# Kernel optimization log

Measured on AMD Instinct MI355X. Metric: run time of the kernel, lower is better.

Reference implementation:

```python
import jax, jax.numpy as jnp
import numpy as np

NUM_CLS = 80
C = 256
IMG = 1024.0
N = 256
SR = 2  # sampling_ratio
MIN_SIZE = 16.0
SCALES = (0.25, 0.125, 0.0625, 0.03125)
HW = ((256, 256), (128, 128), (64, 64), (32, 32))


def _roialign(feat, rois, scale, out):
    # feat: [C, H, W]; rois: [n, 4] (y1, x1, y2, x2) in image coords.
    # torchvision-style ROIAlign (aligned=False), sampling_ratio=SR, avg pool.
    Cc, H, W = feat.shape
    n = rois.shape[0]
    y1 = rois[:, 0] * scale
    x1 = rois[:, 1] * scale
    rh = jnp.maximum(rois[:, 2] * scale - y1, 1.0)
    rw = jnp.maximum(rois[:, 3] * scale - x1, 1.0)
    # per-bin sample offsets: (bin + (s+0.5)/SR) * bin_size
    g = (jnp.arange(out, dtype=feat.dtype)[:, None]
         + (jnp.arange(SR, dtype=feat.dtype)[None, :] + 0.5) / SR).reshape(-1)  # [out*SR]
    ys = y1[:, None] + g[None, :] * (rh / out)[:, None]  # [n, out*SR]
    xs = x1[:, None] + g[None, :] * (rw / out)[:, None]
    S = out * SR
    yy = jnp.broadcast_to(ys[:, :, None], (n, S, S)).reshape(n, S * S)
    xx = jnp.broadcast_to(xs[:, None, :], (n, S, S)).reshape(n, S * S)
    valid = (yy > -1.0) & (yy < H) & (xx > -1.0) & (xx < W)
    yc = jnp.clip(yy, 0.0, H - 1.0)
    xc = jnp.clip(xx, 0.0, W - 1.0)
    y0 = jnp.floor(yc)
    x0 = jnp.floor(xc)
    ly = yc - y0
    lx = xc - x0
    y0i = y0.astype(jnp.int32)
    x0i = x0.astype(jnp.int32)
    y1i = jnp.minimum(y0i + 1, H - 1)
    x1i = jnp.minimum(x0i + 1, W - 1)
    f00 = feat[:, y0i, x0i]  # [C, n, S*S]
    f01 = feat[:, y0i, x1i]
    f10 = feat[:, y1i, x0i]
    f11 = feat[:, y1i, x1i]
    val = (f00 * (1 - ly) * (1 - lx) + f01 * (1 - ly) * lx
           + f10 * ly * (1 - lx) + f11 * ly * lx)
    val = jnp.where(valid[None], val, 0.0)
    val = val.reshape(Cc, n, out, SR, out, SR).mean(axis=(3, 5))
    return val.transpose(1, 0, 2, 3)  # [n, C, out, out]


def _pool(P, rois, out):
    # roi_layer: FPN level assignment via log2 of sqrt(area)/224, clamp to levels 0..3
    area = jnp.prod(rois[:, 2:4] - rois[:, 0:2] + 1.0, axis=-1)
    lvl = jnp.clip(jnp.floor(4.0 + jnp.log(jnp.sqrt(area) / 224.0) / np.log(2.0)), 2.0, 5.0) - 2.0
    lvl = lvl.astype(jnp.int32)
    pooled = jnp.zeros((rois.shape[0], C, out, out), dtype=rois.dtype)
    for l in range(4):
        pl = _roialign(P[l], rois, SCALES[l], out)
        pooled = pooled + jnp.where((lvl == l)[:, None, None, None], pl, 0.0)
    return pooled


def _loc2bbox(loc, anchor):
    chw = anchor[..., 2:4] - anchor[..., 0:2]
    cyx = anchor[..., 0:2] + chw * 0.5
    yx = loc[..., 0:2] * chw + cyx
    hw = jnp.exp(loc[..., 2:4]) * chw
    return jnp.concatenate([yx - hw * 0.5, yx + hw * 0.5], axis=-1)


def _head(x, W1, b1, W2, b2, Wc, bc, Wl, bl):
    x = x.reshape(x.shape[0], -1)
    h = jax.nn.relu(x @ W1 + b1)
    h = jax.nn.relu(h @ W2 + b2)
    return h @ Wc + bc, h @ Wl + bl


def _cascade(P, rois, params):
    stds = (jnp.array([0.1, 0.1, 0.2, 0.2], dtype=rois.dtype),
            jnp.array([0.05, 0.05, 0.1, 0.1], dtype=rois.dtype),
            jnp.array([1 / 30.0, 1 / 30.0, 1 / 15.0, 1 / 15.0], dtype=rois.dtype))
    roi = rois
    valid = jnp.ones((rois.shape[0],), dtype=bool)
    t = jnp.arange(rois.shape[0])
    pre_b = jnp.zeros((rois.shape[0], NUM_CLS, 4), dtype=rois.dtype)
    pre_s = jnp.zeros((rois.shape[0], NUM_CLS), dtype=rois.dtype)
    for s in range(3):
        x = _pool(P, roi, 7)
        logits, loc = _head(x, *params[s])
        loc = loc.reshape(-1, NUM_CLS + 1, 4)[:, 1:] * stds[s]
        boxes = _loc2bbox(loc, roi[:, None, :])  # [N, NUM_CLS, 4]
        score = jax.nn.softmax(logits, axis=-1)[:, 1:]
        pre_b = pre_b + boxes
        pre_s = pre_s + score
        best = jnp.argmax(score, axis=-1)
        roi = boxes[t, best]
        roi = jnp.clip(roi, 0.0, IMG)  # square image: clamp both coords to [0, IMG]
        if s < 2:  # original filters only after stages 1 and 2
            hw = roi[:, 2:4] - roi[:, 0:2]
            valid = valid & jnp.all(hw >= MIN_SIZE, axis=-1)
    m = valid.astype(pre_s.dtype)
    return pre_b / 3.0 * m[:, None, None], pre_s / 3.0 * m[:, None]


def setup_inputs():
    key = jax.random.key(0)
    ks = jax.random.split(key, 32)
    inp = {}
    for i, (h, w) in enumerate(HW):
        inp[f"P{i}"] = jax.random.normal(ks[i], (C, h, w), dtype=jnp.float32)
    yx1 = jax.random.uniform(ks[4], (N, 2), minval=0.0, maxval=IMG - 64.0)
    sz = jnp.exp(jax.random.uniform(ks[5], (N, 2), minval=np.log(16.0), maxval=np.log(600.0)))
    yx2 = jnp.clip(yx1 + sz, 0.0, IMG - 1.0)
    inp["rois"] = jnp.concatenate([yx1, yx2], axis=-1).astype(jnp.float32)
    dims = [(C * 49, 1024), (1024,), (1024, 1024), (1024,),
            (1024, NUM_CLS + 1), (NUM_CLS + 1,), (1024, (NUM_CLS + 1) * 4), ((NUM_CLS + 1) * 4,)]
    names = ["W1", "b1", "W2", "b2", "Wc", "bc", "Wl", "bl"]
    k = 6
    for s in range(3):
        for nm, d in zip(names, dims):
            if len(d) == 1:
                inp[f"s{s}_{nm}"] = jnp.zeros(d, dtype=jnp.float32)
            else:
                inp[f"s{s}_{nm}"] = 0.02 * jax.random.normal(ks[k], d, dtype=jnp.float32)
                k += 1
    return inp


def reference(P0, P1, P2, P3, rois,
              s0_W1, s0_b1, s0_W2, s0_b2, s0_Wc, s0_bc, s0_Wl, s0_bl,
              s1_W1, s1_b1, s1_W2, s1_b2, s1_Wc, s1_bc, s1_Wl, s1_bl,
              s2_W1, s2_b1, s2_W2, s2_b2, s2_Wc, s2_bc, s2_Wl, s2_bl):
    P = (P0, P1, P2, P3)
    params = [(s0_W1, s0_b1, s0_W2, s0_b2, s0_Wc, s0_bc, s0_Wl, s0_bl),
              (s1_W1, s1_b1, s1_W2, s1_b2, s1_Wc, s1_bc, s1_Wl, s1_bl),
              (s2_W1, s2_b1, s2_W2, s2_b2, s2_Wc, s2_bc, s2_Wl, s2_bl)]
    return _cascade(P, rois, params)
```

## Files before the change

kernel.cpp:

```cpp
#include <hip/hip_runtime.h>
#include <math.h>


#define NROI 256
#define NCLS 80
#define APITCH 40

typedef __attribute__((ext_vector_type(8))) short short8;
typedef __attribute__((ext_vector_type(4))) float f32x4;

__device__ __forceinline__ unsigned short f2bf(float f) {
  unsigned u = __builtin_bit_cast(unsigned, f);
  unsigned r = (u + 0x7FFFu + ((u >> 16) & 1u)) >> 16;
  return (unsigned short)r;
}
__device__ __forceinline__ float bf2f(unsigned short u) {
  return __builtin_bit_cast(float, (unsigned)u << 16);
}

__global__ __launch_bounds__(256) void init_kernel(const float* __restrict__ rois,
                                                   float* __restrict__ roi,
                                                   float* __restrict__ valid) {
  int i = blockIdx.x * 256 + threadIdx.x;
  if (i < NROI * 4) roi[i] = rois[i];
  if (i < NROI) valid[i] = 1.0f;
}

__global__ __launch_bounds__(256) void transpose_bf16(const float* __restrict__ W,
                                                      unsigned short* __restrict__ Wt,
                                                      int K, int N) {
  __shared__ unsigned short tile[32][33];
  int t = threadIdx.x;
  int k0 = blockIdx.x * 32;
  int n0 = blockIdx.y * 32;
  int r = t >> 3;
  int c4 = (t & 7) * 4;
  float4 v = *(const float4*)(W + (size_t)(k0 + r) * N + n0 + c4);
  tile[r][c4 + 0] = f2bf(v.x);
  tile[r][c4 + 1] = f2bf(v.y);
  tile[r][c4 + 2] = f2bf(v.z);
  tile[r][c4 + 3] = f2bf(v.w);
  __syncthreads();
  struct __attribute__((aligned(8))) US4 { unsigned short a, b, c, d; } o;
  o.a = tile[c4 + 0][r];
  o.b = tile[c4 + 1][r];
  o.c = tile[c4 + 2][r];
  o.d = tile[c4 + 3][r];
  *(US4*)(Wt + (size_t)(n0 + r) * K + k0 + c4) = o;
}

__global__ __launch_bounds__(256) void transpose_w1(const float* __restrict__ W,
                                                    unsigned short* __restrict__ Wt) {
  __shared__ unsigned short tile[32][33];
  int t = threadIdx.x;
  int kd0 = blockIdx.x * 32;
  int n0 = blockIdx.y * 32;
  int p = kd0 >> 8;
  int c0 = kd0 & 255;
  int r = t >> 3;
  int c4 = (t & 7) * 4;
  int k_src = (c0 + r) * 49 + p;
  float4 v = *(const float4*)(W + (size_t)k_src * 1024 + n0 + c4);
  tile[r][c4 + 0] = f2bf(v.x);
  tile[r][c4 + 1] = f2bf(v.y);
  tile[r][c4 + 2] = f2bf(v.z);
  tile[r][c4 + 3] = f2bf(v.w);
  __syncthreads();
  struct __attribute__((aligned(8))) US4 { unsigned short a, b, c, d; } o;
  o.a = tile[c4 + 0][r];
  o.b = tile[c4 + 1][r];
  o.c = tile[c4 + 2][r];
  o.d = tile[c4 + 3][r];
  *(US4*)(Wt + (size_t)(n0 + r) * 12544 + kd0 + c4) = o;
}

__global__ __launch_bounds__(256) void head_transpose(const float* __restrict__ Wc,
                                                      const float* __restrict__ Wl,
                                                      unsigned short* __restrict__ Wt) {
  __shared__ unsigned short tile[32][33];
  int t = threadIdx.x;
  int k0 = blockIdx.x * 32;
  int n0 = blockIdx.y * 32;
  int r = t >> 3;
  int c4 = (t & 7) * 4;
#pragma unroll
  for (int j = 0; j < 4; j++) {
    int nn = n0 + c4 + j;
    float v = 0.0f;
    if (nn < 81) v = Wc[(size_t)(k0 + r) * 81 + nn];
    else if (nn < 405) v = Wl[(size_t)(k0 + r) * 324 + (nn - 81)];
    tile[r][c4 + j] = f2bf(v);
  }
  __syncthreads();
  struct __attribute__((aligned(8))) US4 { unsigned short a, b, c, d; } o;
  o.a = tile[c4 + 0][r];
  o.b = tile[c4 + 1][r];
  o.c = tile[c4 + 2][r];
  o.d = tile[c4 + 3][r];
  *(US4*)(Wt + (size_t)(n0 + r) * 1024 + k0 + c4) = o;
}

__global__ __launch_bounds__(256) void pool_kernel2(
    const unsigned short* __restrict__ Pb0, const unsigned short* __restrict__ Pb1,
    const unsigned short* __restrict__ Pb2, const unsigned short* __restrict__ Pb3,
    const float* __restrict__ roi, unsigned short* __restrict__ pooled) {
  int t = threadIdx.x;
  int n = blockIdx.y;
  int p = blockIdx.x * 4 + (t >> 6);
  if (p >= 49) return;
  int lane = t & 63;
  int c4 = lane * 4;
  int py = p / 7, px = p % 7;

  float r0 = roi[n * 4 + 0];
  float r1 = roi[n * 4 + 1];
  float r2 = roi[n * 4 + 2];
  float r3 = roi[n * 4 + 3];

  float area = (r2 - r0 + 1.0f) * (r3 - r1 + 1.0f);
  float lf = floorf(4.0f + log2f(sqrtf(area) / 224.0f));
  lf = fminf(fmaxf(lf, 2.0f), 5.0f);
  int lvl = (int)lf - 2;

  float scale;
  int H;
  const unsigned short* fb;
  if (lvl == 0)      { scale = 0.25f;    H = 256; fb = Pb0; }
  else if (lvl == 1) { scale = 0.125f;   H = 128; fb = Pb1; }
  else if (lvl == 2) { scale = 0.0625f;  H = 64;  fb = Pb2; }
  else               { scale = 0.03125f; H = 32;  fb = Pb3; }
  int W = H;

  float y1 = r0 * scale;
  float x1 = r1 * scale;
  float rh = fmaxf(r2 * scale - y1, 1.0f);
  float rw = fmaxf(r3 * scale - x1, 1.0f);
  float bh = rh * (1.0f / 7.0f);
  float bw = rw * (1.0f / 7.0f);

  float a0 = 0.f, a1 = 0.f, a2 = 0.f, a3 = 0.f;
#pragma unroll
  for (int ry = 0; ry < 2; ry++) {
    float yy = y1 + ((float)py + ((float)ry + 0.5f) * 0.5f) * bh;
    bool vy = (yy > -1.0f) && (yy < (float)H);
    float ycl = fminf(fmaxf(yy, 0.0f), (float)(H - 1));
    float y0f = floorf(ycl);
    float ly = ycl - y0f;
    int y0i = (int)y0f;
    int y1i = min(y0i + 1, H - 1);
#pragma unroll
    for (int rx = 0; rx < 2; rx++) {
      float xx = x1 + ((float)px + ((float)rx + 0.5f) * 0.5f) * bw;
      bool vx = (xx > -1.0f) && (xx < (float)W);
      float xcl = fminf(fmaxf(xx, 0.0f), (float)(W - 1));
      float x0f = floorf(xcl);
      float lx = xcl - x0f;
      int x0i = (int)x0f;
      int x1i = min(x0i + 1, W - 1);
      float w00 = (1.f - ly) * (1.f - lx);
      float w01 = (1.f - ly) * lx;
      float w10 = ly * (1.f - lx);
      float w11 = ly * lx;
      if (!(vy && vx)) { w00 = w01 = w10 = w11 = 0.f; }
      ushort4 f00 = *(const ushort4*)(fb + ((size_t)(y0i * W + x0i) * 256 + c4));
      ushort4 f01 = *(const ushort4*)(fb + ((size_t)(y0i * W + x1i) * 256 + c4));
      ushort4 f10 = *(const ushort4*)(fb + ((size_t)(y1i * W + x0i) * 256 + c4));
      ushort4 f11 = *(const ushort4*)(fb + ((size_t)(y1i * W + x1i) * 256 + c4));
      a0 += bf2f(f00.x) * w00 + bf2f(f01.x) * w01 + bf2f(f10.x) * w10 + bf2f(f11.x) * w11;
      a1 += bf2f(f00.y) * w00 + bf2f(f01.y) * w01 + bf2f(f10.y) * w10 + bf2f(f11.y) * w11;
      a2 += bf2f(f00.z) * w00 + bf2f(f01.z) * w01 + bf2f(f10.z) * w10 + bf2f(f11.z) * w11;
      a3 += bf2f(f00.w) * w00 + bf2f(f01.w) * w01 + bf2f(f10.w) * w10 + bf2f(f11.w) * w11;
    }
  }
  ushort4 o;
  o.x = f2bf(a0 * 0.25f);
  o.y = f2bf(a1 * 0.25f);
  o.z = f2bf(a2 * 0.25f);
  o.w = f2bf(a3 * 0.25f);
  *(ushort4*)(pooled + (size_t)n * 12544 + p * 256 + c4) = o;
}

__global__ __launch_bounds__(256) void gemm_bf16(
    const unsigned short* __restrict__ A, const unsigned short* __restrict__ B,
    float* __restrict__ Cpart, int M, int N, int K, int iters) {
  __shared__ unsigned short As[128 * APITCH];
  __shared__ unsigned short Bs[128 * APITCH];
  const int t = threadIdx.x;
  const int n0 = blockIdx.x * 128;
  const int m0 = blockIdx.y * 128;
  const size_t kt0 = (size_t)blockIdx.z * iters * 32;

  const int row = t >> 2;
  const int off = (t & 3) * 8;
  const unsigned short* pa0 = A + (size_t)(m0 + row) * K + kt0 + off;
  const unsigned short* pa1 = pa0 + (size_t)64 * K;
  const unsigned short* pb0 = B + (size_t)(n0 + row) * K + kt0 + off;
  const unsigned short* pb1 = pb0 + (size_t)64 * K;

  const int lane = t & 63;
  const int wave = t >> 6;
  const int wm = (wave >> 1) * 64;
  const int wn = (wave & 1) * 64;
  const int fr = lane & 15;
  const int kq = (lane >> 4) * 8;

  f32x4 acc[4][4];
#pragma unroll
  for (int i = 0; i < 4; i++)
#pragma unroll
    for (int j = 0; j < 4; j++) acc[i][j] = (f32x4){0.f, 0.f, 0.f, 0.f};

  uint4 ra0 = *(const uint4*)pa0;
  uint4 ra1 = *(const uint4*)pa1;
  uint4 rb0 = *(const uint4*)pb0;
  uint4 rb1 = *(const uint4*)pb1;

  for (int it = 0; it < iters; ++it) {
    *(uint4*)&As[row * APITCH + off] = ra0;
    *(uint4*)&As[(row + 64) * APITCH + off] = ra1;
    *(uint4*)&Bs[row * APITCH + off] = rb0;
    *(uint4*)&Bs[(row + 64) * APITCH + off] = rb1;
    __syncthreads();
    if (it + 1 < iters) {
      int d = (it + 1) * 32;
      ra0 = *(const uint4*)(pa0 + d);
      ra1 = *(const uint4*)(pa1 + d);
      rb0 = *(const uint4*)(pb0 + d);
      rb1 = *(const uint4*)(pb1 + d);
    }
    short8 af[4], bfv[4];
#pragma unroll
    for (int f = 0; f < 4; f++)
      af[f] = *(const short8*)&As[(wm + f * 16 + fr) * APITCH + kq];
#pragma unroll
    for (int f = 0; f < 4; f++)
      bfv[f] = *(const short8*)&Bs[(wn + f * 16 + fr) * APITCH + kq];
#pragma unroll
    for (int fm = 0; fm < 4; fm++)
#pragma unroll
      for (int fn = 0; fn < 4; fn++)
        acc[fm][fn] = __builtin_amdgcn_mfma_f32_16x16x32_bf16(af[fm], bfv[fn],
                                                              acc[fm][fn], 0, 0, 0);
    __syncthreads();
  }

  float* Cp = Cpart + (size_t)blockIdx.z * M * N;
  const int colb = n0 + wn + fr;
  const int rowb = m0 + wm + (lane >> 4) * 4;
#pragma unroll
  for (int fm = 0; fm < 4; fm++)
#pragma unroll
    for (int fn = 0; fn < 4; fn++)
#pragma unroll
      for (int r = 0; r < 4; r++)
        Cp[(size_t)(rowb + fm * 16 + r) * N + (colb + fn * 16)] = acc[fm][fn][r];
}

__global__ __launch_bounds__(256) void reduce_bias_relu(
    const float* __restrict__ parts, int nparts, const float* __restrict__ bias,
    unsigned short* __restrict__ outb) {
  int i = blockIdx.x * 256 + threadIdx.x;
  float s = 0.0f;
  for (int p = 0; p < nparts; ++p) s += parts[(size_t)p * 262144 + i];
  s = fmaxf(s + bias[i & 1023], 0.0f);
  outb[i] = f2bf(s);
}

__global__ __launch_bounds__(128) void decode_kernel(
    const float* __restrict__ headp, const float* __restrict__ bc,
    const float* __restrict__ bl,
    float* __restrict__ roi, float* __restrict__ valid,
    float* __restrict__ pre_b, float* __restrict__ pre_s,
    float st0, float st1, float st2, float st3, int stage) {
  int n = blockIdx.x;
  int t = threadIdx.x;
  __shared__ float red[128];
  __shared__ int redi[128];
  __shared__ float sroi[4];
  __shared__ float boxes[NCLS][4];

  if (t < 4) sroi[t] = roi[n * 4 + t];
  float l = -INFINITY;
  if (t < 81) {
    float s = 0.f;
#pragma unroll
    for (int z = 0; z < 4; z++) s += headp[(size_t)z * 131072 + n * 512 + t];
    l = s + bc[t];
  }
  red[t] = l;
  __syncthreads();
#pragma unroll
  for (int s = 64; s > 0; s >>= 1) {
    if (t < s) red[t] = fmaxf(red[t], red[t + s]);
    __syncthreads();
  }
  float mx = red[0];
  __syncthreads();
  red[t] = (t < 81) ? expf(l - mx) : 0.0f;
  __syncthreads();
#pragma unroll
  for (int s = 64; s > 0; s >>= 1) {
    if (t < s) red[t] += red[t + s];
    __syncthreads();
  }
  float denom = red[0];
  __syncthreads();

  float score = -INFINITY;
  if (t < NCLS) {
    float lj = 0.f;
#pragma unroll
    for (int z = 0; z < 4; z++) lj += headp[(size_t)z * 131072 + n * 512 + (t + 1)];
    lj += bc[t + 1];
    score = expf(lj - mx) / denom;
    float lp[4];
#pragma unroll
    for (int j = 0; j < 4; j++) {
      float s = 0.f;
#pragma unroll
      for (int z = 0; z < 4; z++)
        s += headp[(size_t)z * 131072 + n * 512 + 81 + (t + 1) * 4 + j];
      lp[j] = s + bl[(t + 1) * 4 + j];
    }
    float dy = lp[0] * st0;
    float dx = lp[1] * st1;
    float dh = lp[2] * st2;
    float dw = lp[3] * st3;
    float h_ = sroi[2] - sroi[0];
    float w_ = sroi[3] - sroi[1];
    float cy = sroi[0] + h_ * 0.5f;
    float cx = sroi[1] + w_ * 0.5f;
    float ny = dy * h_ + cy;
    float nx = dx * w_ + cx;
    float nh = expf(dh) * h_;
    float nw = expf(dw) * w_;
    float b0 = ny - nh * 0.5f;
    float b1v = nx - nw * 0.5f;
    float b2v = ny + nh * 0.5f;
    float b3v = nx + nw * 0.5f;
    int o = (n * NCLS + t) * 4;
    pre_b[o + 0] += b0;
    pre_b[o + 1] += b1v;
    pre_b[o + 2] += b2v;
    pre_b[o + 3] += b3v;
    pre_s[n * NCLS + t] += score;
    boxes[t][0] = b0;
    boxes[t][1] = b1v;
    boxes[t][2] = b2v;
    boxes[t][3] = b3v;
  }
  red[t] = score;
  redi[t] = t;
  __syncthreads();
  for (int s = 64; s > 0; s >>= 1) {
    if (t < s) {
      float o2 = red[t + s];
      int oi = redi[t + s];
      if (o2 > red[t] || (o2 == red[t] && oi < redi[t])) {
        red[t] = o2;
        redi[t] = oi;
      }
    }
    __syncthreads();
  }
  if (t == 0) {
    int best = redi[0];
    float ry1 = fminf(fmaxf(boxes[best][0], 0.0f), 1024.0f);
    float rx1 = fminf(fmaxf(boxes[best][1], 0.0f), 1024.0f);
    float ry2 = fminf(fmaxf(boxes[best][2], 0.0f), 1024.0f);
    float rx2 = fminf(fmaxf(boxes[best][3], 0.0f), 1024.0f);
    roi[n * 4 + 0] = ry1;
    roi[n * 4 + 1] = rx1;
    roi[n * 4 + 2] = ry2;
    roi[n * 4 + 3] = rx2;
    if (stage < 2) {
      float hh = ry2 - ry1, ww = rx2 - rx1;
      if (!(hh >= 16.0f && ww >= 16.0f)) valid[n] = 0.0f;
    }
  }
}

__global__ __launch_bounds__(256) void finalize_kernel(
    const float* __restrict__ pre_b, const float* __restrict__ pre_s,
    const float* __restrict__ valid, float* __restrict__ out) {
  int i = blockIdx.x * 256 + threadIdx.x;
  if (i < NROI * NCLS * 4) {
    int n = i / (NCLS * 4);
    out[i] = pre_b[i] * valid[n] * (1.0f / 3.0f);
  } else if (i < NROI * NCLS * 4 + NROI * NCLS) {
    int j = i - NROI * NCLS * 4;
    int n = j / NCLS;
    out[i] = pre_s[j] * valid[n] * (1.0f / 3.0f);
  }
}

extern "C" void kernel_launch(void* const* d_in, const int* in_sizes, int n_in,
                              void* d_out, int out_size, void* d_ws, size_t ws_size,
                              hipStream_t stream) {
  const float* P0 = (const float*)d_in[0];
  const float* P1 = (const float*)d_in[1];
  const float* P2 = (const float*)d_in[2];
  const float* P3 = (const float*)d_in[3];
  const float* rois = (const float*)d_in[4];
  float* out = (float*)d_out;
  float* ws = (float*)d_ws;

  float* roi   = ws;
  float* valid = roi + 1024;
  float* pre_b = valid + 256;
  float* pre_s = pre_b + 81920;
  float* part1 = pre_s + 20480;
  float* part2 = part1 + 14 * 262144;
  float* parth = part2 + 8 * 262144;
  unsigned short* pooledb = (unsigned short*)(parth + 4 * 131072);
  unsigned short* Wt1 = pooledb + (size_t)256 * 12544;
  unsigned short* Wt2 = Wt1 + (size_t)1024 * 12544;
  unsigned short* Wth = Wt2 + (size_t)1024 * 1024;
  unsigned short* h1b = Wth + (size_t)512 * 1024;
  unsigned short* h2b = h1b + (size_t)256 * 1024;
  unsigned short* Pb0 = h2b + (size_t)256 * 1024;
  unsigned short* Pb1 = Pb0 + (size_t)65536 * 256;
  unsigned short* Pb2 = Pb1 + (size_t)16384 * 256;
  unsigned short* Pb3 = Pb2 + (size_t)4096 * 256;

  init_kernel<<<4, 256, 0, stream>>>(rois, roi, valid);
  hipMemsetAsync(pre_b, 0, (size_t)(81920 + 20480) * sizeof(float), stream);

  transpose_bf16<<<dim3(8, 2048), 256, 0, stream>>>(P0, Pb0, 256, 65536);
  transpose_bf16<<<dim3(8, 512),  256, 0, stream>>>(P1, Pb1, 256, 16384);
  transpose_bf16<<<dim3(8, 128),  256, 0, stream>>>(P2, Pb2, 256, 4096);
  transpose_bf16<<<dim3(8, 32),   256, 0, stream>>>(P3, Pb3, 256, 1024);

  const float stds[3][4] = {
      {0.1f, 0.1f, 0.2f, 0.2f},
      {0.05f, 0.05f, 0.1f, 0.1f},
      {1.0f / 30.0f, 1.0f / 30.0f, 1.0f / 15.0f, 1.0f / 15.0f}};

  for (int s = 0; s < 3; s++) {
    const float* W1 = (const float*)d_in[5 + s * 8 + 0];
    const float* b1 = (const float*)d_in[5 + s * 8 + 1];
    const float* W2 = (const float*)d_in[5 + s * 8 + 2];
    const float* b2 = (const float*)d_in[5 + s * 8 + 3];
    const float* Wc = (const float*)d_in[5 + s * 8 + 4];
    const float* bc = (const float*)d_in[5 + s * 8 + 5];
    const float* Wl = (const float*)d_in[5 + s * 8 + 6];
    const float* bl = (const float*)d_in[5 + s * 8 + 7];

    transpose_w1<<<dim3(392, 32), 256, 0, stream>>>(W1, Wt1);
    transpose_bf16<<<dim3(32, 32), 256, 0, stream>>>(W2, Wt2, 1024, 1024);
    head_transpose<<<dim3(32, 16), 256, 0, stream>>>(Wc, Wl, Wth);

    pool_kernel2<<<dim3(13, 256), 256, 0, stream>>>(Pb0, Pb1, Pb2, Pb3, roi, pooledb);

    gemm_bf16<<<dim3(8, 2, 14), 256, 0, stream>>>(pooledb, Wt1, part1, 256, 1024, 12544, 28);
    reduce_bias_relu<<<1024, 256, 0, stream>>>(part1, 14, b1, h1b);

    gemm_bf16<<<dim3(8, 2, 8), 256, 0, stream>>>(h1b, Wt2, part2, 256, 1024, 1024, 4);
    reduce_bias_relu<<<1024, 256, 0, stream>>>(part2, 8, b2, h2b);

    gemm_bf16<<<dim3(4, 2, 4), 256, 0, stream>>>(h2b, Wth, parth, 256, 512, 1024, 8);

    decode_kernel<<<256, 128, 0, stream>>>(parth, bc, bl, roi, valid, pre_b, pre_s,
                                           stds[s][0], stds[s][1], stds[s][2], stds[s][3], s);
  }

  finalize_kernel<<<400, 256, 0, stream>>>(pre_b, pre_s, valid, out);
}
```

Before: 505.7 us.

## Batch all weight/feature prep into two kernels and fuse FC2 bias-ReLU epilogue

Hoists the per-stage weight transposes for all three stages into one prep kernel launched up front, together with ROI init and zeroing, and merges the four feature-map transposes into one kernel. This cuts kernel launch count and removes the per-stage serialization of transpose work. The second FC GEMM drops split-K and fuses bias plus ReLU into its epilogue, which removes the partial buffer and a reduce kernel. In exchange, the FC2 GEMM now runs on only 16 blocks with the full K loop, so it exposes much less parallelism, and the workspace must hold three sets of transposed weights.

```diff
diff --git a/kernel.cpp b/kernel.cpp
--- a/kernel.cpp
+++ b/kernel.cpp
@@ -8,6 +8,8 @@
 
 typedef __attribute__((ext_vector_type(8))) short short8;
 typedef __attribute__((ext_vector_type(4))) float f32x4;
+
+struct __attribute__((aligned(8))) US4 { unsigned short a, b, c, d; };
 
 __device__ __forceinline__ unsigned short f2bf(float f) {
   unsigned u = __builtin_bit_cast(unsigned, f);
@@ -18,86 +20,115 @@
   return __builtin_bit_cast(float, (unsigned)u << 16);
 }
 
-__global__ __launch_bounds__(256) void init_kernel(const float* __restrict__ rois,
-                                                   float* __restrict__ roi,
-                                                   float* __restrict__ valid) {
-  int i = blockIdx.x * 256 + threadIdx.x;
-  if (i < NROI * 4) roi[i] = rois[i];
-  if (i < NROI) valid[i] = 1.0f;
-}
-
-__global__ __launch_bounds__(256) void transpose_bf16(const float* __restrict__ W,
-                                                      unsigned short* __restrict__ Wt,
-                                                      int K, int N) {
+struct PrepArgs {
+  const float* W1[3];
+  const float* W2[3];
+  const float* Wc[3];
+  const float* Wl[3];
+  unsigned short* Wt1[3];
+  unsigned short* Wt2[3];
+  unsigned short* Wth[3];
+  const float* rois;
+  float* roi;
+  float* valid;
+  float* zero_base;
+  int zero_count;
+};
+
+__global__ __launch_bounds__(256) void prep_all(PrepArgs a) {
   __shared__ unsigned short tile[32][33];
-  int t = threadIdx.x;
-  int k0 = blockIdx.x * 32;
-  int n0 = blockIdx.y * 32;
+  const int b = blockIdx.x;
+  const int t = threadIdx.x;
+  const int r = t >> 3;
+  const int c4 = (t & 7) * 4;
+
+  if (b < 37632) {
+    int s = b / 12544;
+    int tau = b % 12544;
+    int kd0 = (tau % 392) * 32;
+    int n0 = (tau / 392) * 32;
+    int p = kd0 >> 8;
+    int c0 = kd0 & 255;
+    int k_src = (c0 + r) * 49 + p;
+    float4 v = *(const float4*)(a.W1[s] + (size_t)k_src * 1024 + n0 + c4);
+    tile[r][c4 + 0] = f2bf(v.x);
+    tile[r][c4 + 1] = f2bf(v.y);
+    tile[r][c4 + 2] = f2bf(v.z);
+    tile[r][c4 + 3] = f2bf(v.w);
+    __syncthreads();
+    US4 o = {tile[c4 + 0][r], tile[c4 + 1][r], tile[c4 + 2][r], tile[c4 + 3][r]};
+    *(US4*)(a.Wt1[s] + (size_t)(n0 + r) * 12544 + kd0 + c4) = o;
+  } else if (b < 40704) {
+    int bb = b - 37632;
+    int s = bb / 1024;
+    int tau = bb % 1024;
+    int k0 = (tau % 32) * 32;
+    int n0 = (tau / 32) * 32;
+    float4 v = *(const float4*)(a.W2[s] + (size_t)(k0 + r) * 1024 + n0 + c4);
+    tile[r][c4 + 0] = f2bf(v.x);
+    tile[r][c4 + 1] = f2bf(v.y);
+    tile[r][c4 + 2] = f2bf(v.z);
+    tile[r][c4 + 3] = f2bf(v.w);
+    __syncthreads();
+    US4 o = {tile[c4 + 0][r], tile[c4 + 1][r], tile[c4 + 2][r], tile[c4 + 3][r]};
+    *(US4*)(a.Wt2[s] + (size_t)(n0 + r) * 1024 + k0 + c4) = o;
+  } else if (b < 42240) {
+    int bb = b - 40704;
+    int s = bb / 512;
+    int tau = bb % 512;
+    int k0 = (tau % 32) * 32;
+    int n0 = (tau / 32) * 32;
+#pragma unroll
+    for (int j = 0; j < 4; j++) {
+      int nn = n0 + c4 + j;
+      float v = 0.0f;
+      if (nn < 81) v = a.Wc[s][(size_t)(k0 + r) * 81 + nn];
+      else if (nn < 405) v = a.Wl[s][(size_t)(k0 + r) * 324 + (nn - 81)];
+      tile[r][c4 + j] = f2bf(v);
+    }
+    __syncthreads();
+    US4 o = {tile[c4 + 0][r], tile[c4 + 1][r], tile[c4 + 2][r], tile[c4 + 3][r]};
+    *(US4*)(a.Wth[s] + (size_t)(n0 + r) * 1024 + k0 + c4) = o;
+  } else if (b == 42240) {
+    for (int i = t; i < NROI * 4; i += 256) a.roi[i] = a.rois[i];
+    a.valid[t] = 1.0f;
+  } else {
+    int base = (b - 42241) * 1024 + t;
+#pragma unroll
+    for (int j = 0; j < 4; j++) {
+      int ii = base + j * 256;
+      if (ii < a.zero_count) a.zero_base[ii] = 0.0f;
+    }
+  }
+}
+
+__global__ __launch_bounds__(256) void feat_all(
+    const float* __restrict__ P0, const float* __restrict__ P1,
+    const float* __restrict__ P2, const float* __restrict__ P3,
+    unsigned short* __restrict__ Pb0, unsigned short* __restrict__ Pb1,
+    unsigned short* __restrict__ Pb2, unsigned short* __restrict__ Pb3) {
+  __shared__ unsigned short tile[32][33];
+  const int b = blockIdx.x;
+  const int t = threadIdx.x;
+  const float* src;
+  unsigned short* dst;
+  int N, tau;
+  if (b < 16384)      { src = P0; dst = Pb0; N = 65536; tau = b; }
+  else if (b < 20480) { src = P1; dst = Pb1; N = 16384; tau = b - 16384; }
+  else if (b < 21504) { src = P2; dst = Pb2; N = 4096;  tau = b - 20480; }
+  else                { src = P3; dst = Pb3; N = 1024;  tau = b - 21504; }
+  int k0 = (tau & 7) * 32;
+  int n0 = (tau >> 3) * 32;
   int r = t >> 3;
   int c4 = (t & 7) * 4;
-  float4 v = *(const float4*)(W + (size_t)(k0 + r) * N + n0 + c4);
+  float4 v = *(const float4*)(src + (size_t)(k0 + r) * N + n0 + c4);
   tile[r][c4 + 0] = f2bf(v.x);
   tile[r][c4 + 1] = f2bf(v.y);
   tile[r][c4 + 2] = f2bf(v.z);
   tile[r][c4 + 3] = f2bf(v.w);
   __syncthreads();
-  struct __attribute__((aligned(8))) US4 { unsigned short a, b, c, d; } o;
-  o.a = tile[c4 + 0][r];
-  o.b = tile[c4 + 1][r];
-  o.c = tile[c4 + 2][r];
-  o.d = tile[c4 + 3][r];
-  *(US4*)(Wt + (size_t)(n0 + r) * K + k0 + c4) = o;
-}
-
-__global__ __launch_bounds__(256) void transpose_w1(const float* __restrict__ W,
-                                                    unsigned short* __restrict__ Wt) {
-  __shared__ unsigned short tile[32][33];
-  int t = threadIdx.x;
-  int kd0 = blockIdx.x * 32;
-  int n0 = blockIdx.y * 32;
-  int p = kd0 >> 8;
-  int c0 = kd0 & 255;
-  int r = t >> 3;
-  int c4 = (t & 7) * 4;
-  int k_src = (c0 + r) * 49 + p;
-  float4 v = *(const float4*)(W + (size_t)k_src * 1024 + n0 + c4);
-  tile[r][c4 + 0] = f2bf(v.x);
-  tile[r][c4 + 1] = f2bf(v.y);
-  tile[r][c4 + 2] = f2bf(v.z);
-  tile[r][c4 + 3] = f2bf(v.w);
-  __syncthreads();
-  struct __attribute__((aligned(8))) US4 { unsigned short a, b, c, d; } o;
-  o.a = tile[c4 + 0][r];
-  o.b = tile[c4 + 1][r];
-  o.c = tile[c4 + 2][r];
-  o.d = tile[c4 + 3][r];
-  *(US4*)(Wt + (size_t)(n0 + r) * 12544 + kd0 + c4) = o;
-}
-
-__global__ __launch_bounds__(256) void head_transpose(const float* __restrict__ Wc,
-                                                      const float* __restrict__ Wl,
-                                                      unsigned short* __restrict__ Wt) {
-  __shared__ unsigned short tile[32][33];
-  int t = threadIdx.x;
-  int k0 = blockIdx.x * 32;
-  int n0 = blockIdx.y * 32;
-  int r = t >> 3;
-  int c4 = (t & 7) * 4;
-#pragma unroll
-  for (int j = 0; j < 4; j++) {
-    int nn = n0 + c4 + j;
-    float v = 0.0f;
-    if (nn < 81) v = Wc[(size_t)(k0 + r) * 81 + nn];
-    else if (nn < 405) v = Wl[(size_t)(k0 + r) * 324 + (nn - 81)];
-    tile[r][c4 + j] = f2bf(v);
-  }
-  __syncthreads();
-  struct __attribute__((aligned(8))) US4 { unsigned short a, b, c, d; } o;
-  o.a = tile[c4 + 0][r];
-  o.b = tile[c4 + 1][r];
-  o.c = tile[c4 + 2][r];
-  o.d = tile[c4 + 3][r];
-  *(US4*)(Wt + (size_t)(n0 + r) * 1024 + k0 + c4) = o;
+  US4 o = {tile[c4 + 0][r], tile[c4 + 1][r], tile[c4 + 2][r], tile[c4 + 3][r]};
+  *(US4*)(dst + (size_t)(n0 + r) * 256 + k0 + c4) = o;
 }
 
 __global__ __launch_bounds__(256) void pool_kernel2(
@@ -182,7 +213,8 @@
 
 __global__ __launch_bounds__(256) void gemm_bf16(
     const unsigned short* __restrict__ A, const unsigned short* __restrict__ B,
-    float* __restrict__ Cpart, int M, int N, int K, int iters) {
+    float* __restrict__ Cpart, int M, int N, int K, int iters,
+    const float* __restrict__ bias, unsigned short* __restrict__ fused_out) {
   __shared__ unsigned short As[128 * APITCH];
   __shared__ unsigned short Bs[128 * APITCH];
   const int t = threadIdx.x;
@@ -244,16 +276,31 @@
     __syncthreads();
   }
 
-  float* Cp = Cpart + (size_t)blockIdx.z * M * N;
   const int colb = n0 + wn + fr;
   const int rowb = m0 + wm + (lane >> 4) * 4;
-#pragma unroll
-  for (int fm = 0; fm < 4; fm++)
-#pragma unroll
-    for (int fn = 0; fn < 4; fn++)
-#pragma unroll
-      for (int r = 0; r < 4; r++)
-        Cp[(size_t)(rowb + fm * 16 + r) * N + (colb + fn * 16)] = acc[fm][fn][r];
+  if (fused_out) {
+#pragma unroll
+    for (int fm = 0; fm < 4; fm++)
+#pragma unroll
+      for (int fn = 0; fn < 4; fn++) {
+        int col = colb + fn * 16;
+        float bv = bias[col];
+#pragma unroll
+        for (int r = 0; r < 4; r++) {
+          float v = fmaxf(acc[fm][fn][r] + bv, 0.0f);
+          fused_out[(size_t)(rowb + fm * 16 + r) * N + col] = f2bf(v);
+        }
+      }
+  } else {
+    float* Cp = Cpart + (size_t)blockIdx.z * M * N;
+#pragma unroll
+    for (int fm = 0; fm < 4; fm++)
+#pragma unroll
+      for (int fn = 0; fn < 4; fn++)
+#pragma unroll
+        for (int r = 0; r < 4; r++)
+          Cp[(size_t)(rowb + fm * 16 + r) * N + (colb + fn * 16)] = acc[fm][fn][r];
+  }
 }
 
 __global__ __launch_bounds__(256) void reduce_bias_relu(
@@ -410,26 +457,36 @@
   float* pre_b = valid + 256;
   float* pre_s = pre_b + 81920;
   float* part1 = pre_s + 20480;
-  float* part2 = part1 + 14 * 262144;
-  float* parth = part2 + 8 * 262144;
+  float* parth = part1 + 14 * 262144;
   unsigned short* pooledb = (unsigned short*)(parth + 4 * 131072);
-  unsigned short* Wt1 = pooledb + (size_t)256 * 12544;
-  unsigned short* Wt2 = Wt1 + (size_t)1024 * 12544;
-  unsigned short* Wth = Wt2 + (size_t)1024 * 1024;
-  unsigned short* h1b = Wth + (size_t)512 * 1024;
+  unsigned short* Wt1s = pooledb + (size_t)256 * 12544;
+  unsigned short* Wt2s = Wt1s + (size_t)3 * 1024 * 12544;
+  unsigned short* Wths = Wt2s + (size_t)3 * 1024 * 1024;
+  unsigned short* h1b = Wths + (size_t)3 * 512 * 1024;
   unsigned short* h2b = h1b + (size_t)256 * 1024;
   unsigned short* Pb0 = h2b + (size_t)256 * 1024;
   unsigned short* Pb1 = Pb0 + (size_t)65536 * 256;
   unsigned short* Pb2 = Pb1 + (size_t)16384 * 256;
   unsigned short* Pb3 = Pb2 + (size_t)4096 * 256;
 
-  init_kernel<<<4, 256, 0, stream>>>(rois, roi, valid);
-  hipMemsetAsync(pre_b, 0, (size_t)(81920 + 20480) * sizeof(float), stream);
-
-  transpose_bf16<<<dim3(8, 2048), 256, 0, stream>>>(P0, Pb0, 256, 65536);
-  transpose_bf16<<<dim3(8, 512),  256, 0, stream>>>(P1, Pb1, 256, 16384);
-  transpose_bf16<<<dim3(8, 128),  256, 0, stream>>>(P2, Pb2, 256, 4096);
-  transpose_bf16<<<dim3(8, 32),   256, 0, stream>>>(P3, Pb3, 256, 1024);
+  PrepArgs pa;
+  for (int s = 0; s < 3; s++) {
+    pa.W1[s] = (const float*)d_in[5 + s * 8 + 0];
+    pa.W2[s] = (const float*)d_in[5 + s * 8 + 2];
+    pa.Wc[s] = (const float*)d_in[5 + s * 8 + 4];
+    pa.Wl[s] = (const float*)d_in[5 + s * 8 + 6];
+    pa.Wt1[s] = Wt1s + (size_t)s * 1024 * 12544;
+    pa.Wt2[s] = Wt2s + (size_t)s * 1024 * 1024;
+    pa.Wth[s] = Wths + (size_t)s * 512 * 1024;
+  }
+  pa.rois = rois;
+  pa.roi = roi;
+  pa.valid = valid;
+  pa.zero_base = pre_b;
+  pa.zero_count = 81920 + 20480;
+
+  feat_all<<<21760, 256, 0, stream>>>(P0, P1, P2, P3, Pb0, Pb1, Pb2, Pb3);
+  prep_all<<<42341, 256, 0, stream>>>(pa);
 
   const float stds[3][4] = {
       {0.1f, 0.1f, 0.2f, 0.2f},
@@ -437,28 +494,22 @@
       {1.0f / 30.0f, 1.0f / 30.0f, 1.0f / 15.0f, 1.0f / 15.0f}};
 
   for (int s = 0; s < 3; s++) {
-    const float* W1 = (const float*)d_in[5 + s * 8 + 0];
     const float* b1 = (const float*)d_in[5 + s * 8 + 1];
-    const float* W2 = (const float*)d_in[5 + s * 8 + 2];
     const float* b2 = (const float*)d_in[5 + s * 8 + 3];
-    const float* Wc = (const float*)d_in[5 + s * 8 + 4];
     const float* bc = (const float*)d_in[5 + s * 8 + 5];
-    const float* Wl = (const float*)d_in[5 + s * 8 + 6];
     const float* bl = (const float*)d_in[5 + s * 8 + 7];
 
-    transpose_w1<<<dim3(392, 32), 256, 0, stream>>>(W1, Wt1);
-    transpose_bf16<<<dim3(32, 32), 256, 0, stream>>>(W2, Wt2, 1024, 1024);
-    head_transpose<<<dim3(32, 16), 256, 0, stream>>>(Wc, Wl, Wth);
-
     pool_kernel2<<<dim3(13, 256), 256, 0, stream>>>(Pb0, Pb1, Pb2, Pb3, roi, pooledb);
 
-    gemm_bf16<<<dim3(8, 2, 14), 256, 0, stream>>>(pooledb, Wt1, part1, 256, 1024, 12544, 28);
+    gemm_bf16<<<dim3(8, 2, 14), 256, 0, stream>>>(
+        pooledb, pa.Wt1[s], part1, 256, 1024, 12544, 28, nullptr, nullptr);
     reduce_bias_relu<<<1024, 256, 0, stream>>>(part1, 14, b1, h1b);
 
-    gemm_bf16<<<dim3(8, 2, 8), 256, 0, stream>>>(h1b, Wt2, part2, 256, 1024, 1024, 4);
-    reduce_bias_relu<<<1024, 256, 0, stream>>>(part2, 8, b2, h2b);
-
-    gemm_bf16<<<dim3(4, 2, 4), 256, 0, stream>>>(h2b, Wth, parth, 256, 512, 1024, 8);
+    gemm_bf16<<<dim3(8, 2, 1), 256, 0, stream>>>(
+        h1b, pa.Wt2[s], nullptr, 256, 1024, 1024, 32, b2, h2b);
+
+    gemm_bf16<<<dim3(4, 2, 4), 256, 0, stream>>>(
+        h2b, pa.Wth[s], parth, 256, 512, 1024, 8, nullptr, nullptr);
 
     decode_kernel<<<256, 128, 0, stream>>>(parth, bc, bl, roi, valid, pre_b, pre_s,
                                            stds[s][0], stds[s][1], stds[s][2], stds[s][3], s);
```

Result: slower. 516.9 us (+2.2%).
